# Kernel optimization log

Measured on AMD Instinct MI355X. Metric: run time of the kernel, lower is better.

## Reference

```python
import jax, jax.numpy as jnp
import numpy as np

B, N, HS, NH = 32, 256, 768, 32
D = HS // NH  # 24


def setup_inputs() -> dict:
    key = jax.random.key(0)
    ks = jax.random.split(key, 20)
    s = 0.02
    inp = {
        "hidden_states": jax.random.normal(ks[0], (B, N, HS), jnp.float32),
        "attention_bias": jax.random.normal(ks[1], (B, NH, N, N), jnp.float32),
        "delta_pos": jax.random.normal(ks[2], (B, N, N, 3), jnp.float32),
        "attention_mask": jnp.ones((B, N), jnp.float32),
        "Wi": jax.random.normal(ks[3], (HS, HS), jnp.float32) * s,
        "bi": jnp.zeros((HS,), jnp.float32),
        "Wq": jax.random.normal(ks[4], (HS, HS), jnp.float32) * s,
        "bq": jnp.zeros((HS,), jnp.float32),
        "Wk": jax.random.normal(ks[5], (HS, HS), jnp.float32) * s,
        "bk": jnp.zeros((HS,), jnp.float32),
        "Wv": jax.random.normal(ks[6], (HS, HS), jnp.float32) * s,
        "bv": jnp.zeros((HS,), jnp.float32),
        "Wf1": jax.random.normal(ks[7], (1, HS), jnp.float32) * s,
        "bf1": jnp.zeros((1,), jnp.float32),
        "Wf2": jax.random.normal(ks[8], (1, HS), jnp.float32) * s,
        "bf2": jnp.zeros((1,), jnp.float32),
        "Wf3": jax.random.normal(ks[9], (1, HS), jnp.float32) * s,
        "bf3": jnp.zeros((1,), jnp.float32),
    }
    return inp


def reference(hidden_states, attention_bias, delta_pos, attention_mask,
              Wi, bi, Wq, bq, Wk, bk, Wv, bv, Wf1, bf1, Wf2, bf2, Wf3, bf3):
    b, n, hs = hidden_states.shape
    nh = NH
    d = hs // nh
    denoise_scaling = d ** (-0.5)
    scale = np.sqrt(denoise_scaling).astype(np.float32)

    # mask: (B,N) -> additive (B,1,1,N)
    neg = ((1.0 - attention_mask) * -100000.0)[:, None, None, :]

    h = jax.nn.gelu(hidden_states @ Wi.T + bi, approximate=False)
    q = (h @ Wq.T + bq).reshape(b, n, nh, d).transpose(0, 2, 1, 3) * scale
    k = (h @ Wk.T + bk).reshape(b, n, nh, d).transpose(0, 2, 1, 3) * scale
    v = (h @ Wv.T + bv).reshape(b, n, nh, d).transpose(0, 2, 1, 3)

    scores = jnp.einsum('bhid,bhjd->bhij', q, k) + attention_bias + neg
    probs = jax.nn.softmax(scores, axis=-1)  # dropout = identity at eval

    # x[b,i,c,h,d] = sum_j probs[b,h,i,j] * delta_pos[b,i,j,c] * v[b,h,j,d]
    x = jnp.einsum('bhij,bijc,bhjd->bichd', probs, delta_pos, v)
    x = x.reshape(b, n, 3, hs)

    f1 = x[:, :, 0, :] @ Wf1.T + bf1  # (B,N,1)
    f2 = x[:, :, 1, :] @ Wf2.T + bf2
    f3 = x[:, :, 2, :] @ Wf3.T + bf3
    return jnp.concatenate([f1, f2, f3], axis=-1).astype(jnp.float32)
```

## Files before the change

### kernel.cpp

```cpp
#include <hip/hip_runtime.h>
#include <hip/hip_fp16.h>

#define B_  32
#define N_  256
#define HS_ 768
#define NH_ 32
#define D_  24
#define M_  (B_*N_)
#define QKVN 2304

typedef unsigned short us8 __attribute__((ext_vector_type(8)));
typedef unsigned short us4v __attribute__((ext_vector_type(4)));
typedef _Float16 f16x8 __attribute__((ext_vector_type(8)));
typedef float f32x4 __attribute__((ext_vector_type(4)));

__device__ __forceinline__ unsigned short f2h(float x){
  return __half_as_ushort(__float2half(x));
}
__device__ __forceinline__ float h2f(unsigned short u){
  return __half2float(__ushort_as_half(u));
}
__device__ __forceinline__ void gload16(const void* g, void* l){
  __builtin_amdgcn_global_load_lds(
      (const __attribute__((address_space(1))) void*)g,
      (__attribute__((address_space(3))) void*)l, 16, 0, 0);
}
__device__ __forceinline__ void pin4(float4 &v){
  asm volatile("" : "+v"(v.x), "+v"(v.y), "+v"(v.z), "+v"(v.w));
}

__global__ __launch_bounds__(256) void cvt_kernel(const float* __restrict__ in,
                                                  unsigned short* __restrict__ out, int n4){
  int i = blockIdx.x*256 + threadIdx.x;
  if (i >= n4) return;
  float4 v = ((const float4*)in)[i];
  ushort4 o;
  o.x = f2h(v.x); o.y = f2h(v.y); o.z = f2h(v.z); o.w = f2h(v.w);
  ((ushort4*)out)[i] = o;
}

__global__ __launch_bounds__(256) void gemm128_kernel(
    const unsigned short* __restrict__ A, const unsigned short* __restrict__ W,
    const float* __restrict__ b0, const float* __restrict__ b1, const float* __restrict__ b2,
    unsigned short* __restrict__ C, int M, int N, int K, int dogelu, int headmajor)
{
  __shared__ unsigned short As[128*64];
  __shared__ unsigned short Bs[128*64];
  int gswz = blockIdx.x;
  int chunkg = gridDim.x >> 3;
  int bid = (gswz & 7)*chunkg + (gswz >> 3);
  int tid = threadIdx.x;
  int nT = N >> 7;
  int tm = bid / nT;
  int tn = bid - tm*nT;
  int which = (tn << 7) / 768;
  const float* bp = (which == 0) ? b0 : (which == 1) ? b1 : b2;
  bp -= which * 768;
  int wave = tid >> 6, lane = tid & 63;
  int wm = (wave >> 1) << 6;
  int wn = (wave & 1) << 6;
  int fr = lane & 15;
  int g  = lane >> 4;

  size_t aoff[4], woff[4];
  int ldsb[4];
#pragma unroll
  for (int s4 = 0; s4 < 4; s4++){
    int ob = s4*4096 + tid*16;
    int r  = ob >> 7;
    int p  = (ob >> 4) & 7;
    int l  = p ^ (r & 7);
    aoff[s4] = ((size_t)(tm*128 + r)*K)*2 + l*16;
    woff[s4] = ((size_t)(tn*128 + r)*K)*2 + l*16;
    ldsb[s4] = s4*4096 + wave*1024;
  }
  const char* Ab = (const char*)A;
  const char* Wb = (const char*)W;
  char* AsB = (char*)As;
  char* BsB = (char*)Bs;

  f32x4 acc[4][4];
#pragma unroll
  for (int m = 0; m < 4; m++)
#pragma unroll
    for (int n = 0; n < 4; n++) acc[m][n] = (f32x4){0.f,0.f,0.f,0.f};

  for (int k0 = 0; k0 < K; k0 += 64){
    size_t kb = (size_t)k0*2;
#pragma unroll
    for (int s4 = 0; s4 < 4; s4++) gload16(Ab + aoff[s4] + kb, AsB + ldsb[s4]);
#pragma unroll
    for (int s4 = 0; s4 < 4; s4++) gload16(Wb + woff[s4] + kb, BsB + ldsb[s4]);
    __syncthreads();

    f16x8 af[4], bf[4];
#pragma unroll
    for (int m = 0; m < 4; m++){
      int row = wm + m*16 + fr;
      af[m] = __builtin_bit_cast(f16x8, *(const us8*)(AsB + row*128 + ((g ^ (row & 7))*16)));
    }
#pragma unroll
    for (int n = 0; n < 4; n++){
      int row = wn + n*16 + fr;
      bf[n] = __builtin_bit_cast(f16x8, *(const us8*)(BsB + row*128 + ((g ^ (row & 7))*16)));
    }
#pragma unroll
    for (int m = 0; m < 4; m++)
#pragma unroll
      for (int n = 0; n < 4; n++)
        acc[m][n] = __builtin_amdgcn_mfma_f32_16x16x32_f16(af[m], bf[n], acc[m][n], 0, 0, 0);

#pragma unroll
    for (int m = 0; m < 4; m++){
      int row = wm + m*16 + fr;
      af[m] = __builtin_bit_cast(f16x8, *(const us8*)(AsB + row*128 + (((g+4) ^ (row & 7))*16)));
    }
#pragma unroll
    for (int n = 0; n < 4; n++){
      int row = wn + n*16 + fr;
      bf[n] = __builtin_bit_cast(f16x8, *(const us8*)(BsB + row*128 + (((g+4) ^ (row & 7))*16)));
    }
#pragma unroll
    for (int m = 0; m < 4; m++)
#pragma unroll
      for (int n = 0; n < 4; n++)
        acc[m][n] = __builtin_amdgcn_mfma_f32_16x16x32_f16(af[m], bf[n], acc[m][n], 0, 0, 0);
    __syncthreads();
  }

#pragma unroll
  for (int n = 0; n < 4; n++){
    int col = tn*128 + wn + n*16 + fr;
    float bv = bp[col];
    int mat = col / 768;
    int hd  = col - mat*768;
    int hh  = hd / 24;
    int dd  = hd - hh*24;
#pragma unroll
    for (int m = 0; m < 4; m++){
      int row = tm*128 + wm + m*16 + g*4;
      size_t hmbase = ((size_t)(mat*1024 + (row >> 8)*32 + hh))*6144 + (row & 255)*24 + dd;
#pragma unroll
      for (int q = 0; q < 4; q++){
        float v = acc[m][n][q] + bv;
        if (dogelu) v = 0.5f*v*(1.0f + erff(v*0.70710678118654752f));
        if (headmajor) C[hmbase + q*24] = f2h(v);
        else           C[(size_t)(row + q)*N + col] = f2h(v);
      }
    }
  }
}

__global__ __launch_bounds__(256) void prep_kernel(
    const unsigned short* __restrict__ qkvh, const float* __restrict__ mask,
    const float* __restrict__ Wf1, const float* __restrict__ Wf2, const float* __restrict__ Wf3,
    unsigned short* __restrict__ u16,
    float* __restrict__ negv)
{
  int bh = blockIdx.x;
  int h = bh & 31, b = bh >> 5;
  int j = threadIdx.x;
  const unsigned short* vr = qkvh + ((size_t)(2*1024 + b*32 + h))*6144 + j*24;
  us8 v0 = *(const us8*)(vr);
  us8 v1 = *(const us8*)(vr + 8);
  us8 v2 = *(const us8*)(vr + 16);
  const float* w1 = Wf1 + h*D_;
  const float* w2 = Wf2 + h*D_;
  const float* w3 = Wf3 + h*D_;
  float u0 = 0.f, u1 = 0.f, u2 = 0.f;
#pragma unroll
  for (int e = 0; e < 8; e++){
    float va = h2f(v0[e]), vb2 = h2f(v1[e]), vc = h2f(v2[e]);
    u0 += va*w1[e] + vb2*w1[8+e] + vc*w1[16+e];
    u1 += va*w2[e] + vb2*w2[8+e] + vc*w2[16+e];
    u2 += va*w3[e] + vb2*w3[8+e] + vc*w3[16+e];
  }
  us4v o = {f2h(u0), f2h(u1), f2h(u2), 0};
  *(us4v*)(u16 + ((size_t)bh*N_ + j)*4) = o;
  if (h == 0) negv[b*N_ + j] = (1.0f - mask[b*N_ + j]) * -100000.0f;
}

#define SCALE 0.20412414523193154f
#define INVSCALE 4.898979485566356f
#define M0 16.0f
__global__ __launch_bounds__(256, 4) void attn_kernel(
    const unsigned short* __restrict__ qkvh,
    const float* __restrict__ bias,
    const unsigned short* __restrict__ u16,
    const float* __restrict__ negv,
    const float* __restrict__ dp,
    float* __restrict__ fpart)
{
  int gswz = blockIdx.x;
  int lin = (gswz & 7)*128 + (gswz >> 3);
  int b = lin >> 5, ic = (lin >> 1) & 15, jh = lin & 1;
  int i0 = ic*16, j00 = jh*128;
  int t = threadIdx.x;
  int wave = t >> 6, lane = t & 63;
  int ch = wave, fr = lane & 15, g = lane >> 4;

  __shared__ __align__(16) char smem[35840];
  char* zp = smem + 32768;
  char* scratch = smem + 33792;

  int bsrc[2];
#pragma unroll
  for (int k = 0; k < 2; k++){
    int a = k*4096 + t*16;
    int row = a >> 9;
    int pc = (a >> 4) & 31;
    int lc = pc ^ (row & 7);
    bsrc[k] = row*1024 + lc*16;
  }
  const char* bb0 = (const char*)bias
      + ((size_t)(b*NH_)*65536 + (size_t)i0*256 + j00)*4;

  const char* qkvhB = (const char*)qkvh;
  const char* kbase0 = qkvhB + ((size_t)(1024 + b*32))*12288 + jh*6144;
  const char* qbase0 = qkvhB + ((size_t)(b*32))*12288 + (size_t)i0*48;
  const char* ubase0 = (const char*)u16 + ((size_t)(b*NH_))*2048 + jh*1024;
  const char* sbase[2]; int sstep[2];
#pragma unroll
  for (int k = 0; k < 2; k++){
    int G = k*256 + t;
    if (G < 384){ sbase[k] = kbase0 + G*16;        sstep[k] = 12288; }
    else if (G < 432){ sbase[k] = qbase0 + (G-384)*16; sstep[k] = 12288; }
    else if (G < 496){ sbase[k] = ubase0 + (G-432)*16; sstep[k] = 2048; }
    else { sbase[k] = ubase0; sstep[k] = 2048; }
  }

  #define ISSUE(hh) do { \
    int _par = (hh) & 1; \
    const char* _bp = bb0 + (size_t)(hh)*262144; \
    gload16(_bp + bsrc[0], smem + _par*8192 + wave*1024); \
    gload16(_bp + bsrc[1], smem + _par*8192 + 4096 + wave*1024); \
    gload16(sbase[0] + (size_t)(hh)*sstep[0], smem + 16384 + _par*8192 + wave*1024); \
    gload16(sbase[1] + (size_t)(hh)*sstep[1], smem + 16384 + _par*8192 + 4096 + wave*1024); \
  } while(0)

  float4 nv[2]; float4 dpre[6];
  {
    const float* nb = negv + b*N_ + j00;
#pragma unroll
    for (int jt = 0; jt < 2; jt++)
      nv[jt] = *(const float4*)(nb + ch*32 + jt*16 + g*4);
    const float* dpb = dp + (size_t)(b*N_ + i0 + fr)*768;
#pragma unroll
    for (int jt = 0; jt < 2; jt++){
      const float4* dq = (const float4*)(dpb + (size_t)(j00 + ch*32 + jt*16 + g*4)*3);
      dpre[jt*3+0] = dq[0]; dpre[jt*3+1] = dq[1]; dpre[jt*3+2] = dq[2];
    }
  }
  asm volatile("s_waitcnt vmcnt(0)" ::: "memory");
  pin4(nv[0]); pin4(nv[1]);
#pragma unroll
  for (int k = 0; k < 6; k++) pin4(dpre[k]);

  ISSUE(0);
  gload16(negv + b*N_, scratch);
  if (t < 128) *(us8*)(zp + t*16) = (us8){0,0,0,0,0,0,0,0};
  asm volatile("s_waitcnt lgkmcnt(0)" ::: "memory");

  int swz = (fr & 7) << 4;
  float4* fp4 = (float4*)fpart;
  size_t fbase = (((size_t)(b*16 + ic)*2 + jh)*32)*64 + ch*16 + fr;

#pragma unroll 1
  for (int h = 0; h < 32; h++){
    asm volatile("s_waitcnt vmcnt(1)" ::: "memory");
    __builtin_amdgcn_s_barrier();
    if (h < 31) ISSUE(h+1);

    const char* bslot = smem + (h & 1)*8192;
    const char* sslot = smem + 16384 + (h & 1)*8192;

    const char* qa = (g < 3) ? (sslot + 6144 + fr*48 + g*16) : (zp + fr*16);
    f16x8 qf = __builtin_bit_cast(f16x8, *(const us8*)qa);

    float S = 0.f, a0 = 0.f, a1 = 0.f, a2 = 0.f;
#pragma unroll
    for (int jt = 0; jt < 2; jt++){
      int j0l = ch*32 + jt*16 + g*4;
      float4 bv = *(const float4*)(bslot + fr*512 + ((j0l*4) ^ swz));
      f32x4 cin;
      cin[0] = (bv.x + nv[jt].x)*INVSCALE;
      cin[1] = (bv.y + nv[jt].y)*INVSCALE;
      cin[2] = (bv.z + nv[jt].z)*INVSCALE;
      cin[3] = (bv.w + nv[jt].w)*INVSCALE;
      int krow = ch*32 + jt*16 + fr;
      const char* ka = sslot + krow*48 + g*16;
      f16x8 kf = __builtin_bit_cast(f16x8, *(const us8*)ka);
      f32x4 sv = __builtin_amdgcn_mfma_f32_16x16x32_f16(kf, qf, cin, 0, 0, 0);
      float p0 = __expf(fmaf(sv[0], SCALE, -M0));
      float p1 = __expf(fmaf(sv[1], SCALE, -M0));
      float p2 = __expf(fmaf(sv[2], SCALE, -M0));
      float p3 = __expf(fmaf(sv[3], SCALE, -M0));
      S += p0 + p1 + p2 + p3;
      us8 ua = *(const us8*)(sslot + 6912 + j0l*8);
      us8 ub = *(const us8*)(sslot + 6912 + j0l*8 + 16);
      float4 d0 = dpre[jt*3], d1 = dpre[jt*3+1], d2 = dpre[jt*3+2];
      a0 += p0*h2f(ua[0])*d0.x + p1*h2f(ua[4])*d0.w + p2*h2f(ub[0])*d1.z + p3*h2f(ub[4])*d2.y;
      a1 += p0*h2f(ua[1])*d0.y + p1*h2f(ua[5])*d1.x + p2*h2f(ub[1])*d1.w + p3*h2f(ub[5])*d2.z;
      a2 += p0*h2f(ua[2])*d0.z + p1*h2f(ua[6])*d1.y + p2*h2f(ub[2])*d2.x + p3*h2f(ub[6])*d2.w;
    }
    S  += __shfl_xor(S, 16);  S  += __shfl_xor(S, 32);
    a0 += __shfl_xor(a0, 16); a0 += __shfl_xor(a0, 32);
    a1 += __shfl_xor(a1, 16); a1 += __shfl_xor(a1, 32);
    a2 += __shfl_xor(a2, 16); a2 += __shfl_xor(a2, 32);
    if (lane < 16)
      fp4[fbase + (size_t)h*64] = make_float4(S, a0, a1, a2);
  }
  asm volatile("s_waitcnt vmcnt(0)" ::: "memory");
  #undef ISSUE
}

__global__ __launch_bounds__(256) void final_kernel(const float* __restrict__ fpart,
    const float* __restrict__ bf1, const float* __restrict__ bf2, const float* __restrict__ bf3,
    float* __restrict__ out)
{
  int idx = blockIdx.x*256 + threadIdx.x;
  int b = idx >> 8, i = idx & 255;
  int ic = i >> 4, ii = i & 15;
  const float4* fp4 = (const float4*)fpart;
  size_t base = ((size_t)(b*16 + ic)*2)*2048 + ii;
  float acc0 = 0.f, acc1 = 0.f, acc2 = 0.f;
#pragma unroll 4
  for (int h = 0; h < 32; h++){
    float S = 0.f, A0 = 0.f, A1 = 0.f, A2 = 0.f;
#pragma unroll
    for (int jh = 0; jh < 2; jh++){
#pragma unroll
      for (int ch = 0; ch < 4; ch++){
        float4 v = fp4[base + (size_t)jh*2048 + (size_t)h*64 + ch*16];
        S += v.x; A0 += v.y; A1 += v.z; A2 += v.w;
      }
    }
    float rs = 1.0f / S;
    acc0 += A0*rs; acc1 += A1*rs; acc2 += A2*rs;
  }
  float* op = out + (size_t)idx*3;
  op[0] = acc0 + bf1[0];
  op[1] = acc1 + bf2[0];
  op[2] = acc2 + bf3[0];
}

extern "C" void kernel_launch(void* const* d_in, const int* in_sizes, int n_in,
                              void* d_out, int out_size, void* d_ws, size_t ws_size,
                              hipStream_t stream)
{
  const float* X    = (const float*)d_in[0];
  const float* bias = (const float*)d_in[1];
  const float* dp   = (const float*)d_in[2];
  const float* mask = (const float*)d_in[3];
  const float* Wi   = (const float*)d_in[4];
  const float* bi   = (const float*)d_in[5];
  const float* Wq   = (const float*)d_in[6];
  const float* bq   = (const float*)d_in[7];
  const float* Wk   = (const float*)d_in[8];
  const float* bk   = (const float*)d_in[9];
  const float* Wv   = (const float*)d_in[10];
  const float* bv   = (const float*)d_in[11];
  const float* Wf1  = (const float*)d_in[12];
  const float* bf1  = (const float*)d_in[13];
  const float* Wf2  = (const float*)d_in[14];
  const float* bf2  = (const float*)d_in[15];
  const float* Wf3  = (const float*)d_in[16];
  const float* bf3  = (const float*)d_in[17];
  float* out = (float*)d_out;

  unsigned short* xb   = (unsigned short*)d_ws;
  unsigned short* wib  = xb   + (size_t)M_*HS_;
  unsigned short* wqb  = wib  + (size_t)HS_*HS_;
  unsigned short* wkb  = wqb  + (size_t)HS_*HS_;
  unsigned short* wvb  = wkb  + (size_t)HS_*HS_;
  unsigned short* hb   = wvb  + (size_t)HS_*HS_;
  unsigned short* qkvh = hb   + (size_t)M_*HS_;
  unsigned short* u16a = qkvh + (size_t)3*1024*6144;
  float* negv  = (float*)(u16a + (size_t)B_*NH_*N_*4);
  float* fpart = negv + (size_t)B_*N_;

  {
    int n4 = M_*HS_/4;
    cvt_kernel<<<n4/256, 256, 0, stream>>>(X, xb, n4);
    int w4 = HS_*HS_/4;
    cvt_kernel<<<w4/256, 256, 0, stream>>>(Wi, wib, w4);
    cvt_kernel<<<w4/256, 256, 0, stream>>>(Wq, wqb, w4);
    cvt_kernel<<<w4/256, 256, 0, stream>>>(Wk, wkb, w4);
    cvt_kernel<<<w4/256, 256, 0, stream>>>(Wv, wvb, w4);
  }

  gemm128_kernel<<<(M_/128)*(HS_/128), 256, 0, stream>>>(xb, wib, bi, bi, bi, hb, M_, HS_, HS_, 1, 0);
  gemm128_kernel<<<(M_/128)*(QKVN/128), 256, 0, stream>>>(hb, wqb, bq, bk, bv, qkvh, M_, QKVN, HS_, 0, 1);

  prep_kernel<<<B_*NH_, 256, 0, stream>>>(qkvh, mask, Wf1, Wf2, Wf3, u16a, negv);

  attn_kernel<<<B_*16*2, 256, 0, stream>>>(qkvh, bias, u16a, negv, dp, fpart);

  final_kernel<<<(B_*N_)/256, 256, 0, stream>>>(fpart, bf1, bf2, bf3, out);
}
```

Baseline: 183.7 us.

## Triple-buffer bias loads in attention and move head-major reshape out of GEMM

The QKV GEMM now writes a plain row-major output, and a separate reshape kernel scatters Q and K into head-major layout while also computing the V projections onto Wf. The attention kernel now triple-buffers the bias tile, issuing it two heads ahead with the side data one head ahead. It also reads its zero padding from a global zero buffer instead of zeroing shared memory. The aims are to avoid the scattered 2-byte stores in the GEMM epilogue and to hide bias-load latency, at the cost of an extra pass over the QKV tensor and more shared memory per block.

```diff
diff --git a/kernel.cpp b/kernel.cpp
--- a/kernel.cpp
+++ b/kernel.cpp
@@ -42,7 +42,7 @@
 __global__ __launch_bounds__(256) void gemm128_kernel(
     const unsigned short* __restrict__ A, const unsigned short* __restrict__ W,
     const float* __restrict__ b0, const float* __restrict__ b1, const float* __restrict__ b2,
-    unsigned short* __restrict__ C, int M, int N, int K, int dogelu, int headmajor)
+    unsigned short* __restrict__ C, int M, int N, int K, int dogelu)
 {
   __shared__ unsigned short As[128*64];
   __shared__ unsigned short Bs[128*64];
@@ -132,38 +132,38 @@
   for (int n = 0; n < 4; n++){
     int col = tn*128 + wn + n*16 + fr;
     float bv = bp[col];
-    int mat = col / 768;
-    int hd  = col - mat*768;
-    int hh  = hd / 24;
-    int dd  = hd - hh*24;
 #pragma unroll
     for (int m = 0; m < 4; m++){
       int row = tm*128 + wm + m*16 + g*4;
-      size_t hmbase = ((size_t)(mat*1024 + (row >> 8)*32 + hh))*6144 + (row & 255)*24 + dd;
 #pragma unroll
       for (int q = 0; q < 4; q++){
         float v = acc[m][n][q] + bv;
         if (dogelu) v = 0.5f*v*(1.0f + erff(v*0.70710678118654752f));
-        if (headmajor) C[hmbase + q*24] = f2h(v);
-        else           C[(size_t)(row + q)*N + col] = f2h(v);
+        C[(size_t)(row + q)*N + col] = f2h(v);
       }
     }
   }
 }
 
-__global__ __launch_bounds__(256) void prep_kernel(
-    const unsigned short* __restrict__ qkvh, const float* __restrict__ mask,
+__global__ __launch_bounds__(256) void reshape_kernel(
+    const unsigned short* __restrict__ qkv, const float* __restrict__ mask,
     const float* __restrict__ Wf1, const float* __restrict__ Wf2, const float* __restrict__ Wf3,
+    unsigned short* __restrict__ qkvh,
     unsigned short* __restrict__ u16,
-    float* __restrict__ negv)
+    float* __restrict__ negv,
+    unsigned short* __restrict__ zws)
 {
   int bh = blockIdx.x;
   int h = bh & 31, b = bh >> 5;
-  int j = threadIdx.x;
-  const unsigned short* vr = qkvh + ((size_t)(2*1024 + b*32 + h))*6144 + j*24;
-  us8 v0 = *(const us8*)(vr);
-  us8 v1 = *(const us8*)(vr + 8);
-  us8 v2 = *(const us8*)(vr + 16);
+  int n = threadIdx.x;
+  const unsigned short* src = qkv + (size_t)(b*N_ + n)*QKVN + h*D_;
+  us8 q0 = *(const us8*)(src),      q1 = *(const us8*)(src+8),    q2 = *(const us8*)(src+16);
+  us8 k0 = *(const us8*)(src+768),  k1 = *(const us8*)(src+776),  k2 = *(const us8*)(src+784);
+  us8 v0 = *(const us8*)(src+1536), v1 = *(const us8*)(src+1544), v2 = *(const us8*)(src+1552);
+  unsigned short* qd = qkvh + (size_t)bh*6144 + n*24;
+  *(us8*)(qd) = q0; *(us8*)(qd+8) = q1; *(us8*)(qd+16) = q2;
+  unsigned short* kd = qkvh + (size_t)(1024 + bh)*6144 + n*24;
+  *(us8*)(kd) = k0; *(us8*)(kd+8) = k1; *(us8*)(kd+16) = k2;
   const float* w1 = Wf1 + h*D_;
   const float* w2 = Wf2 + h*D_;
   const float* w3 = Wf3 + h*D_;
@@ -176,8 +176,9 @@
     u2 += va*w3[e] + vb2*w3[8+e] + vc*w3[16+e];
   }
   us4v o = {f2h(u0), f2h(u1), f2h(u2), 0};
-  *(us4v*)(u16 + ((size_t)bh*N_ + j)*4) = o;
-  if (h == 0) negv[b*N_ + j] = (1.0f - mask[b*N_ + j]) * -100000.0f;
+  *(us4v*)(u16 + ((size_t)bh*N_ + n)*4) = o;
+  if (h == 0) negv[b*N_ + n] = (1.0f - mask[b*N_ + n]) * -100000.0f;
+  if (bh == 0 && n < 32) ((us4v*)zws)[n] = (us4v){0,0,0,0};
 }
 
 #define SCALE 0.20412414523193154f
@@ -189,6 +190,7 @@
     const unsigned short* __restrict__ u16,
     const float* __restrict__ negv,
     const float* __restrict__ dp,
+    const unsigned short* __restrict__ zws,
     float* __restrict__ fpart)
 {
   int gswz = blockIdx.x;
@@ -199,9 +201,7 @@
   int wave = t >> 6, lane = t & 63;
   int ch = wave, fr = lane & 15, g = lane >> 4;
 
-  __shared__ __align__(16) char smem[35840];
-  char* zp = smem + 32768;
-  char* scratch = smem + 33792;
+  __shared__ __align__(16) char smem[40960];
 
   int bsrc[2];
 #pragma unroll
@@ -219,23 +219,25 @@
   const char* kbase0 = qkvhB + ((size_t)(1024 + b*32))*12288 + jh*6144;
   const char* qbase0 = qkvhB + ((size_t)(b*32))*12288 + (size_t)i0*48;
   const char* ubase0 = (const char*)u16 + ((size_t)(b*NH_))*2048 + jh*1024;
-  const char* sbase[2]; int sstep[2];
+  const char* sbase[2]; size_t sstep[2];
 #pragma unroll
   for (int k = 0; k < 2; k++){
     int G = k*256 + t;
-    if (G < 384){ sbase[k] = kbase0 + G*16;        sstep[k] = 12288; }
+    if (G < 384){ sbase[k] = kbase0 + G*16;            sstep[k] = 12288; }
     else if (G < 432){ sbase[k] = qbase0 + (G-384)*16; sstep[k] = 12288; }
     else if (G < 496){ sbase[k] = ubase0 + (G-432)*16; sstep[k] = 2048; }
-    else { sbase[k] = ubase0; sstep[k] = 2048; }
-  }
-
-  #define ISSUE(hh) do { \
+    else { sbase[k] = (const char*)zws + (G-496)*16;   sstep[k] = 0; }
+  }
+
+  #define ISSUE_BIAS(hh, slot) do { \
+    const char* _bp = bb0 + (size_t)((hh) & 31)*262144; \
+    gload16(_bp + bsrc[0], smem + (slot)*8192 + wave*1024); \
+    gload16(_bp + bsrc[1], smem + (slot)*8192 + 4096 + wave*1024); \
+  } while(0)
+  #define ISSUE_SIDE(hh) do { \
     int _par = (hh) & 1; \
-    const char* _bp = bb0 + (size_t)(hh)*262144; \
-    gload16(_bp + bsrc[0], smem + _par*8192 + wave*1024); \
-    gload16(_bp + bsrc[1], smem + _par*8192 + 4096 + wave*1024); \
-    gload16(sbase[0] + (size_t)(hh)*sstep[0], smem + 16384 + _par*8192 + wave*1024); \
-    gload16(sbase[1] + (size_t)(hh)*sstep[1], smem + 16384 + _par*8192 + 4096 + wave*1024); \
+    gload16(sbase[0] + (size_t)((hh) & 31)*sstep[0], smem + 24576 + _par*8192 + wave*1024); \
+    gload16(sbase[1] + (size_t)((hh) & 31)*sstep[1], smem + 24576 + _par*8192 + 4096 + wave*1024); \
   } while(0)
 
   float4 nv[2]; float4 dpre[6];
@@ -256,10 +258,10 @@
 #pragma unroll
   for (int k = 0; k < 6; k++) pin4(dpre[k]);
 
-  ISSUE(0);
-  gload16(negv + b*N_, scratch);
-  if (t < 128) *(us8*)(zp + t*16) = (us8){0,0,0,0,0,0,0,0};
-  asm volatile("s_waitcnt lgkmcnt(0)" ::: "memory");
+  ISSUE_BIAS(0, 0);
+  ISSUE_SIDE(0);
+  ISSUE_BIAS(1, 1);
+  gload16(zws, smem + 24576 + 8192 + 7936);
 
   int swz = (fr & 7) << 4;
   float4* fp4 = (float4*)fpart;
@@ -267,12 +269,17 @@
 
 #pragma unroll 1
   for (int h = 0; h < 32; h++){
-    asm volatile("s_waitcnt vmcnt(1)" ::: "memory");
+    asm volatile("s_waitcnt vmcnt(3)" ::: "memory");
     __builtin_amdgcn_s_barrier();
-    if (h < 31) ISSUE(h+1);
-
-    const char* bslot = smem + (h & 1)*8192;
-    const char* sslot = smem + 16384 + (h & 1)*8192;
+    ISSUE_SIDE(h + 1);
+    {
+      int s2 = (h + 2) % 3;
+      ISSUE_BIAS(h + 2, s2);
+    }
+
+    const char* bslot = smem + (h % 3)*8192;
+    const char* sslot = smem + 24576 + (h & 1)*8192;
+    const char* zp = sslot + 7936;
 
     const char* qa = (g < 3) ? (sslot + 6144 + fr*48 + g*16) : (zp + fr*16);
     f16x8 qf = __builtin_bit_cast(f16x8, *(const us8*)qa);
@@ -311,7 +318,8 @@
       fp4[fbase + (size_t)h*64] = make_float4(S, a0, a1, a2);
   }
   asm volatile("s_waitcnt vmcnt(0)" ::: "memory");
-  #undef ISSUE
+  #undef ISSUE_BIAS
+  #undef ISSUE_SIDE
 }
 
 __global__ __launch_bounds__(256) void final_kernel(const float* __restrict__ fpart,
@@ -374,10 +382,12 @@
   unsigned short* wkb  = wqb  + (size_t)HS_*HS_;
   unsigned short* wvb  = wkb  + (size_t)HS_*HS_;
   unsigned short* hb   = wvb  + (size_t)HS_*HS_;
-  unsigned short* qkvh = hb   + (size_t)M_*HS_;
-  unsigned short* u16a = qkvh + (size_t)3*1024*6144;
+  unsigned short* qkvb = hb   + (size_t)M_*HS_;
+  unsigned short* qkvh = qkvb + (size_t)M_*QKVN;
+  unsigned short* u16a = qkvh + (size_t)2*1024*6144;
   float* negv  = (float*)(u16a + (size_t)B_*NH_*N_*4);
-  float* fpart = negv + (size_t)B_*N_;
+  unsigned short* zws = (unsigned short*)(negv + (size_t)B_*N_);
+  float* fpart = (float*)(zws + 256);
 
   {
     int n4 = M_*HS_/4;
@@ -389,12 +399,12 @@
     cvt_kernel<<<w4/256, 256, 0, stream>>>(Wv, wvb, w4);
   }
 
-  gemm128_kernel<<<(M_/128)*(HS_/128), 256, 0, stream>>>(xb, wib, bi, bi, bi, hb, M_, HS_, HS_, 1, 0);
-  gemm128_kernel<<<(M_/128)*(QKVN/128), 256, 0, stream>>>(hb, wqb, bq, bk, bv, qkvh, M_, QKVN, HS_, 0, 1);
-
-  prep_kernel<<<B_*NH_, 256, 0, stream>>>(qkvh, mask, Wf1, Wf2, Wf3, u16a, negv);
-
-  attn_kernel<<<B_*16*2, 256, 0, stream>>>(qkvh, bias, u16a, negv, dp, fpart);
+  gemm128_kernel<<<(M_/128)*(HS_/128), 256, 0, stream>>>(xb, wib, bi, bi, bi, hb, M_, HS_, HS_, 1);
+  gemm128_kernel<<<(M_/128)*(QKVN/128), 256, 0, stream>>>(hb, wqb, bq, bk, bv, qkvb, M_, QKVN, HS_, 0);
+
+  reshape_kernel<<<B_*NH_, 256, 0, stream>>>(qkvb, mask, Wf1, Wf2, Wf3, qkvh, u16a, negv, zws);
+
+  attn_kernel<<<B_*16*2, 256, 0, stream>>>(qkvh, bias, u16a, negv, dp, zws, fpart);
 
   final_kernel<<<(B_*N_)/256, 256, 0, stream>>>(fpart, bf1, bf2, bf3, out);
 }
```

Result: slower. 206.5 us (+12.4%).

## Fold V projection into Wf weights, drop prep kernel, use exp2

Applied to the files above, without the earlier changes.

Precomputes the product of Wv with the Wf1/Wf2/Wf3 vectors (padded to 128 rows) so the QKV GEMM computes the per-head u values directly instead of a full V projection. This shrinks the second GEMM from 2304 to 1664 output columns and removes the prep kernel and the V write/read. The mask is now turned into the additive term inside the attention kernel, and exp is replaced by a raw v_exp_f32 with pre-scaled log2 constants. The change adds a small weight-prep kernel, gives a slightly different fp16 rounding path for u, and relies on the mask being folded correctly.

```diff
diff --git a/kernel.cpp b/kernel.cpp
--- a/kernel.cpp
+++ b/kernel.cpp
@@ -7,7 +7,7 @@
 #define NH_ 32
 #define D_  24
 #define M_  (B_*N_)
-#define QKVN 2304
+#define NQKU 1664
 
 typedef unsigned short us8 __attribute__((ext_vector_type(8)));
 typedef unsigned short us4v __attribute__((ext_vector_type(4)));
@@ -27,6 +27,9 @@
 }
 __device__ __forceinline__ void pin4(float4 &v){
   asm volatile("" : "+v"(v.x), "+v"(v.y), "+v"(v.z), "+v"(v.w));
+}
+__device__ __forceinline__ float fexp2(float x){
+  float r; asm("v_exp_f32 %0, %1" : "=v"(r) : "v"(x)); return r;
 }
 
 __global__ __launch_bounds__(256) void cvt_kernel(const float* __restrict__ in,
@@ -39,10 +42,44 @@
   ((ushort4*)out)[i] = o;
 }
 
+__global__ __launch_bounds__(256) void wuprep_kernel(
+    const float* __restrict__ Wv, const float* __restrict__ bvv,
+    const float* __restrict__ Wf1, const float* __restrict__ Wf2, const float* __restrict__ Wf3,
+    unsigned short* __restrict__ wu,
+    float* __restrict__ bu)
+{
+  int r = blockIdx.x;
+  unsigned short* dst = wu + (size_t)r*768;
+  int k = threadIdx.x;
+  if (r < 96){
+    int c = r >> 5, h = r & 31;
+    const float* wf = (c == 0 ? Wf1 : c == 1 ? Wf2 : Wf3) + h*D_;
+    float wfl[24];
+#pragma unroll
+    for (int d = 0; d < 24; d++) wfl[d] = wf[d];
+    for (int kk = k; kk < 768; kk += 256){
+      float s = 0.f;
+#pragma unroll
+      for (int d = 0; d < 24; d++) s += wfl[d]*Wv[(size_t)(h*24 + d)*768 + kk];
+      dst[kk] = f2h(s);
+    }
+    if (k == 0){
+      float s = 0.f;
+      for (int d = 0; d < 24; d++) s += bvv[h*24 + d]*wfl[d];
+      bu[r] = s;
+    }
+  } else {
+    for (int kk = k; kk < 768; kk += 256) dst[kk] = 0;
+    if (k == 0) bu[r] = 0.f;
+  }
+}
+
 __global__ __launch_bounds__(256) void gemm128_kernel(
     const unsigned short* __restrict__ A, const unsigned short* __restrict__ W,
     const float* __restrict__ b0, const float* __restrict__ b1, const float* __restrict__ b2,
-    unsigned short* __restrict__ C, int M, int N, int K, int dogelu, int headmajor)
+    unsigned short* __restrict__ C, unsigned short* __restrict__ qkvh,
+    unsigned short* __restrict__ u16,
+    int M, int N, int K, int dogelu, int mode)
 {
   __shared__ unsigned short As[128*64];
   __shared__ unsigned short Bs[128*64];
@@ -53,9 +90,6 @@
   int nT = N >> 7;
   int tm = bid / nT;
   int tn = bid - tm*nT;
-  int which = (tn << 7) / 768;
-  const float* bp = (which == 0) ? b0 : (which == 1) ? b1 : b2;
-  bp -= which * 768;
   int wave = tid >> 6, lane = tid & 63;
   int wm = (wave >> 1) << 6;
   int wn = (wave & 1) << 6;
@@ -128,66 +162,76 @@
     __syncthreads();
   }
 
-#pragma unroll
-  for (int n = 0; n < 4; n++){
-    int col = tn*128 + wn + n*16 + fr;
-    float bv = bp[col];
-    int mat = col / 768;
-    int hd  = col - mat*768;
-    int hh  = hd / 24;
-    int dd  = hd - hh*24;
-#pragma unroll
-    for (int m = 0; m < 4; m++){
-      int row = tm*128 + wm + m*16 + g*4;
-      size_t hmbase = ((size_t)(mat*1024 + (row >> 8)*32 + hh))*6144 + (row & 255)*24 + dd;
-#pragma unroll
-      for (int q = 0; q < 4; q++){
-        float v = acc[m][n][q] + bv;
-        if (dogelu) v = 0.5f*v*(1.0f + erff(v*0.70710678118654752f));
-        if (headmajor) C[hmbase + q*24] = f2h(v);
-        else           C[(size_t)(row + q)*N + col] = f2h(v);
+  if (mode == 0){
+    const float* bp = b0;
+#pragma unroll
+    for (int n = 0; n < 4; n++){
+      int col = tn*128 + wn + n*16 + fr;
+      float bv = bp[col];
+#pragma unroll
+      for (int m = 0; m < 4; m++){
+        int row = tm*128 + wm + m*16 + g*4;
+#pragma unroll
+        for (int q = 0; q < 4; q++){
+          float v = acc[m][n][q] + bv;
+          if (dogelu) v = 0.5f*v*(1.0f + erff(v*0.70710678118654752f));
+          C[(size_t)(row + q)*N + col] = f2h(v);
+        }
       }
     }
-  }
-}
-
-__global__ __launch_bounds__(256) void prep_kernel(
-    const unsigned short* __restrict__ qkvh, const float* __restrict__ mask,
-    const float* __restrict__ Wf1, const float* __restrict__ Wf2, const float* __restrict__ Wf3,
-    unsigned short* __restrict__ u16,
-    float* __restrict__ negv)
-{
-  int bh = blockIdx.x;
-  int h = bh & 31, b = bh >> 5;
-  int j = threadIdx.x;
-  const unsigned short* vr = qkvh + ((size_t)(2*1024 + b*32 + h))*6144 + j*24;
-  us8 v0 = *(const us8*)(vr);
-  us8 v1 = *(const us8*)(vr + 8);
-  us8 v2 = *(const us8*)(vr + 16);
-  const float* w1 = Wf1 + h*D_;
-  const float* w2 = Wf2 + h*D_;
-  const float* w3 = Wf3 + h*D_;
-  float u0 = 0.f, u1 = 0.f, u2 = 0.f;
-#pragma unroll
-  for (int e = 0; e < 8; e++){
-    float va = h2f(v0[e]), vb2 = h2f(v1[e]), vc = h2f(v2[e]);
-    u0 += va*w1[e] + vb2*w1[8+e] + vc*w1[16+e];
-    u1 += va*w2[e] + vb2*w2[8+e] + vc*w2[16+e];
-    u2 += va*w3[e] + vb2*w3[8+e] + vc*w3[16+e];
-  }
-  us4v o = {f2h(u0), f2h(u1), f2h(u2), 0};
-  *(us4v*)(u16 + ((size_t)bh*N_ + j)*4) = o;
-  if (h == 0) negv[b*N_ + j] = (1.0f - mask[b*N_ + j]) * -100000.0f;
+  } else {
+    int which = (tn < 6) ? 0 : (tn < 12) ? 1 : 2;
+    if (which < 2){
+      const float* bp = which ? (b1 - 768) : b0;
+#pragma unroll
+      for (int n = 0; n < 4; n++){
+        int col = tn*128 + wn + n*16 + fr;
+        float bv = bp[col];
+        int hd = col - which*768;
+        int hh = hd / 24;
+        int dd = hd - hh*24;
+#pragma unroll
+        for (int m = 0; m < 4; m++){
+          int row = tm*128 + wm + m*16 + g*4;
+          size_t hmbase = ((size_t)(which*1024 + (row >> 8)*32 + hh))*6144 + (row & 255)*24 + dd;
+#pragma unroll
+          for (int q = 0; q < 4; q++)
+            qkvh[hmbase + q*24] = f2h(acc[m][n][q] + bv);
+        }
+      }
+    } else {
+#pragma unroll
+      for (int n = 0; n < 4; n++){
+        int col = tn*128 + wn + n*16 + fr;
+        int cu = col - 1536;
+        if (cu < 96){
+          int c = cu >> 5, hh = cu & 31;
+          float bv = b2[cu];
+#pragma unroll
+          for (int m = 0; m < 4; m++){
+            int row = tm*128 + wm + m*16 + g*4;
+            int bb = row >> 8, nr = row & 255;
+            unsigned short* ud = u16 + ((size_t)(bb*32 + hh)*256 + nr)*4 + c;
+#pragma unroll
+            for (int q = 0; q < 4; q++)
+              ud[q*4] = f2h(acc[m][n][q] + bv);
+          }
+        }
+      }
+    }
+  }
 }
 
 #define SCALE 0.20412414523193154f
 #define INVSCALE 4.898979485566356f
-#define M0 16.0f
+#define SL2 0.2944888918959693f
+#define ML2 -23.083120654223414f
+#define NEGS (100000.0f*INVSCALE)
 __global__ __launch_bounds__(256, 4) void attn_kernel(
     const unsigned short* __restrict__ qkvh,
     const float* __restrict__ bias,
     const unsigned short* __restrict__ u16,
-    const float* __restrict__ negv,
+    const float* __restrict__ mask,
     const float* __restrict__ dp,
     float* __restrict__ fpart)
 {
@@ -219,11 +263,11 @@
   const char* kbase0 = qkvhB + ((size_t)(1024 + b*32))*12288 + jh*6144;
   const char* qbase0 = qkvhB + ((size_t)(b*32))*12288 + (size_t)i0*48;
   const char* ubase0 = (const char*)u16 + ((size_t)(b*NH_))*2048 + jh*1024;
-  const char* sbase[2]; int sstep[2];
+  const char* sbase[2]; size_t sstep[2];
 #pragma unroll
   for (int k = 0; k < 2; k++){
     int G = k*256 + t;
-    if (G < 384){ sbase[k] = kbase0 + G*16;        sstep[k] = 12288; }
+    if (G < 384){ sbase[k] = kbase0 + G*16;            sstep[k] = 12288; }
     else if (G < 432){ sbase[k] = qbase0 + (G-384)*16; sstep[k] = 12288; }
     else if (G < 496){ sbase[k] = ubase0 + (G-432)*16; sstep[k] = 2048; }
     else { sbase[k] = ubase0; sstep[k] = 2048; }
@@ -238,12 +282,17 @@
     gload16(sbase[1] + (size_t)(hh)*sstep[1], smem + 16384 + _par*8192 + 4096 + wave*1024); \
   } while(0)
 
-  float4 nv[2]; float4 dpre[6];
+  float4 nvs[2]; float4 dpre[6];
   {
-    const float* nb = negv + b*N_ + j00;
-#pragma unroll
-    for (int jt = 0; jt < 2; jt++)
-      nv[jt] = *(const float4*)(nb + ch*32 + jt*16 + g*4);
+    const float* mb = mask + b*N_ + j00;
+#pragma unroll
+    for (int jt = 0; jt < 2; jt++){
+      float4 m4 = *(const float4*)(mb + ch*32 + jt*16 + g*4);
+      nvs[jt].x = fmaf(m4.x, NEGS, -NEGS);
+      nvs[jt].y = fmaf(m4.y, NEGS, -NEGS);
+      nvs[jt].z = fmaf(m4.z, NEGS, -NEGS);
+      nvs[jt].w = fmaf(m4.w, NEGS, -NEGS);
+    }
     const float* dpb = dp + (size_t)(b*N_ + i0 + fr)*768;
 #pragma unroll
     for (int jt = 0; jt < 2; jt++){
@@ -252,12 +301,12 @@
     }
   }
   asm volatile("s_waitcnt vmcnt(0)" ::: "memory");
-  pin4(nv[0]); pin4(nv[1]);
+  pin4(nvs[0]); pin4(nvs[1]);
 #pragma unroll
   for (int k = 0; k < 6; k++) pin4(dpre[k]);
 
   ISSUE(0);
-  gload16(negv + b*N_, scratch);
+  gload16(mask + b*N_, scratch);
   if (t < 128) *(us8*)(zp + t*16) = (us8){0,0,0,0,0,0,0,0};
   asm volatile("s_waitcnt lgkmcnt(0)" ::: "memory");
 
@@ -283,18 +332,18 @@
       int j0l = ch*32 + jt*16 + g*4;
       float4 bv = *(const float4*)(bslot + fr*512 + ((j0l*4) ^ swz));
       f32x4 cin;
-      cin[0] = (bv.x + nv[jt].x)*INVSCALE;
-      cin[1] = (bv.y + nv[jt].y)*INVSCALE;
-      cin[2] = (bv.z + nv[jt].z)*INVSCALE;
-      cin[3] = (bv.w + nv[jt].w)*INVSCALE;
+      cin[0] = fmaf(bv.x, INVSCALE, nvs[jt].x);
+      cin[1] = fmaf(bv.y, INVSCALE, nvs[jt].y);
+      cin[2] = fmaf(bv.z, INVSCALE, nvs[jt].z);
+      cin[3] = fmaf(bv.w, INVSCALE, nvs[jt].w);
       int krow = ch*32 + jt*16 + fr;
       const char* ka = sslot + krow*48 + g*16;
       f16x8 kf = __builtin_bit_cast(f16x8, *(const us8*)ka);
       f32x4 sv = __builtin_amdgcn_mfma_f32_16x16x32_f16(kf, qf, cin, 0, 0, 0);
-      float p0 = __expf(fmaf(sv[0], SCALE, -M0));
-      float p1 = __expf(fmaf(sv[1], SCALE, -M0));
-      float p2 = __expf(fmaf(sv[2], SCALE, -M0));
-      float p3 = __expf(fmaf(sv[3], SCALE, -M0));
+      float p0 = fexp2(fmaf(sv[0], SL2, ML2));
+      float p1 = fexp2(fmaf(sv[1], SL2, ML2));
+      float p2 = fexp2(fmaf(sv[2], SL2, ML2));
+      float p3 = fexp2(fmaf(sv[3], SL2, ML2));
       S += p0 + p1 + p2 + p3;
       us8 ua = *(const us8*)(sslot + 6912 + j0l*8);
       us8 ub = *(const us8*)(sslot + 6912 + j0l*8 + 16);
@@ -370,31 +419,30 @@
 
   unsigned short* xb   = (unsigned short*)d_ws;
   unsigned short* wib  = xb   + (size_t)M_*HS_;
-  unsigned short* wqb  = wib  + (size_t)HS_*HS_;
-  unsigned short* wkb  = wqb  + (size_t)HS_*HS_;
-  unsigned short* wvb  = wkb  + (size_t)HS_*HS_;
-  unsigned short* hb   = wvb  + (size_t)HS_*HS_;
+  unsigned short* wqk  = wib  + (size_t)HS_*HS_;
+  unsigned short* hb   = wqk  + (size_t)NQKU*HS_;
   unsigned short* qkvh = hb   + (size_t)M_*HS_;
-  unsigned short* u16a = qkvh + (size_t)3*1024*6144;
-  float* negv  = (float*)(u16a + (size_t)B_*NH_*N_*4);
-  float* fpart = negv + (size_t)B_*N_;
+  unsigned short* u16a = qkvh + (size_t)2*1024*6144;
+  float* bu    = (float*)(u16a + (size_t)B_*NH_*N_*4);
+  float* fpart = bu + 128;
 
   {
     int n4 = M_*HS_/4;
     cvt_kernel<<<n4/256, 256, 0, stream>>>(X, xb, n4);
     int w4 = HS_*HS_/4;
     cvt_kernel<<<w4/256, 256, 0, stream>>>(Wi, wib, w4);
-    cvt_kernel<<<w4/256, 256, 0, stream>>>(Wq, wqb, w4);
-    cvt_kernel<<<w4/256, 256, 0, stream>>>(Wk, wkb, w4);
-    cvt_kernel<<<w4/256, 256, 0, stream>>>(Wv, wvb, w4);
-  }
-
-  gemm128_kernel<<<(M_/128)*(HS_/128), 256, 0, stream>>>(xb, wib, bi, bi, bi, hb, M_, HS_, HS_, 1, 0);
-  gemm128_kernel<<<(M_/128)*(QKVN/128), 256, 0, stream>>>(hb, wqb, bq, bk, bv, qkvh, M_, QKVN, HS_, 0, 1);
-
-  prep_kernel<<<B_*NH_, 256, 0, stream>>>(qkvh, mask, Wf1, Wf2, Wf3, u16a, negv);
-
-  attn_kernel<<<B_*16*2, 256, 0, stream>>>(qkvh, bias, u16a, negv, dp, fpart);
+    cvt_kernel<<<w4/256, 256, 0, stream>>>(Wq, wqk, w4);
+    cvt_kernel<<<w4/256, 256, 0, stream>>>(Wk, wqk + (size_t)768*768, w4);
+    wuprep_kernel<<<128, 256, 0, stream>>>(Wv, bv, Wf1, Wf2, Wf3,
+                                           wqk + (size_t)1536*768, bu);
+  }
+
+  gemm128_kernel<<<(M_/128)*(HS_/128), 256, 0, stream>>>(
+      xb, wib, bi, bi, bi, hb, hb, u16a, M_, HS_, HS_, 1, 0);
+  gemm128_kernel<<<(M_/128)*(NQKU/128), 256, 0, stream>>>(
+      hb, wqk, bq, bk, bu, hb, qkvh, u16a, M_, NQKU, HS_, 0, 1);
+
+  attn_kernel<<<B_*16*2, 256, 0, stream>>>(qkvh, bias, u16a, mask, dp, fpart);
 
   final_kernel<<<(B_*N_)/256, 256, 0, stream>>>(fpart, bf1, bf2, bf3, out);
 }
```

Result: faster. 180.0 us (-2.0%).
